# Optimization experiments

Hardware: AMD Instinct MI355X
Metric: run time of the kernel (lower is better)

## Reference

```python
import math
import jax, jax.numpy as jnp
import numpy as np

EPS = 1e-7
MAX_TANH_ARG = 1.0 - 1e-5

def _norm(x):
    return jnp.sqrt(jnp.sum(x * x, axis=-1, keepdims=True)).clip(EPS)

def logmap0(x):  # Poincare ball, c=1
    n = _norm(x)
    return jnp.arctanh(jnp.clip(n, EPS, MAX_TANH_ARG)) * x / n

def expmap0(v):
    n = _norm(v)
    return jnp.tanh(n) * v / n

def mobius_add(x, y):
    x2 = jnp.sum(x * x, -1, keepdims=True)
    y2 = jnp.sum(y * y, -1, keepdims=True)
    xy = jnp.sum(x * y, -1, keepdims=True)
    num = (1 + 2 * xy + y2) * x + (1 - x2) * y
    den = (1 + 2 * xy + x2 * y2).clip(EPS)
    return num / den

def plin(x, w, b):  # PoincareLinear: tangent-space affine map
    return expmap0(logmap0(x) @ w + b)

def layer_norm(x, eps=1e-6):  # elementwise_affine=False
    m = x.mean(-1, keepdims=True)
    v = ((x - m) ** 2).mean(-1, keepdims=True)
    return (x - m) / jnp.sqrt(v + eps)

def _beta(a, b):
    return math.exp(math.lgamma(a) + math.lgamma(b) - math.lgamma(a + b))

D, H, FF = 1024, 16, 4096
HD = D // H
BETA_N = _beta(D / 2, 0.5)   # beta(n/2, 1/2) for full dim
BETA_H = _beta(HD / 2, 0.5)  # beta(ni/2, 1/2) for head dim


def setup_inputs() -> dict:
    key = jax.random.key(0)
    ks = jax.random.split(key, 20)
    B, S = 4, 1024
    x = expmap0(0.02 * jax.random.normal(ks[0], (B, S, D), jnp.float32))
    t_emb = jax.random.normal(ks[1], (B, 1, D), jnp.float32)
    g = lambda k, sh: 0.02 * jax.random.normal(k, sh, jnp.float32)
    return {
        'x': x, 't_emb': t_emb,
        'w_q': g(ks[2], (D, D)), 'b_q': jnp.zeros((D,), jnp.float32),
        'w_k': g(ks[3], (D, D)), 'b_k': jnp.zeros((D,), jnp.float32),
        'w_v': g(ks[4], (D, D)), 'b_v': jnp.zeros((D,), jnp.float32),
        'w_o': g(ks[5], (D, D)), 'b_o': jnp.zeros((D,), jnp.float32),
        'w_f1': g(ks[6], (D, FF)), 'b_f1': jnp.zeros((FF,), jnp.float32),
        'w_f2': g(ks[7], (FF, D)), 'b_f2': jnp.zeros((D,), jnp.float32),
        'w_ada': g(ks[8], (D, 6 * D)), 'b_ada': jnp.zeros((6 * D,), jnp.float32),
    }


def _to_heads(p):
    # beta-split: logmap0, split per head, scale by beta_ni/beta_n, expmap0
    B, S, _ = p.shape
    t = logmap0(p).reshape(B, S, H, HD) * (BETA_H / BETA_N)
    return expmap0(jnp.transpose(t, (0, 2, 1, 3)))  # [B,H,S,HD]


def _from_heads(ph):
    # beta-concat: logmap0 per head, scale by beta_n/beta_ni, concat, expmap0
    B, _, S, _ = ph.shape
    t = logmap0(ph) * (BETA_N / BETA_H)
    t = jnp.transpose(t, (0, 2, 1, 3)).reshape(B, S, D)
    return expmap0(t)


def reference(x, t_emb, w_q, b_q, w_k, b_k, w_v, b_v, w_o, b_o,
              w_f1, b_f1, w_f2, b_f2, w_ada, b_ada):
    ada = t_emb @ w_ada + b_ada  # [B,1,6D]
    sh_msa, sc_msa, g_msa, sh_mlp, sc_mlp, g_mlp = jnp.split(ada, 6, axis=-1)

    # --- attention block ---
    residual = x
    xn = layer_norm(logmap0(x))
    xm = expmap0(xn * (1 + sc_msa) + sh_msa)

    q = _to_heads(plin(xm, w_q, b_q))
    k = _to_heads(plin(xm, w_k, b_k))
    v = _to_heads(plin(xm, w_v, b_v))

    qt, kt, vt = logmap0(q), logmap0(k), logmap0(v)
    scores = jnp.einsum('bhqd,bhkd->bhqk', qt, kt) / math.sqrt(HD)
    attn = jax.nn.softmax(scores, axis=-1)
    out_h = expmap0(jnp.einsum('bhqk,bhkd->bhqd', attn, vt))  # [B,H,S,HD]

    attn_out = plin(_from_heads(out_h), w_o, b_o)
    attn_t = g_msa * logmap0(attn_out)
    x = mobius_add(residual, expmap0(attn_t))

    # --- FFN block ---
    residual = x
    xn = layer_norm(logmap0(x))
    xm = expmap0(xn * (1 + sc_mlp) + sh_mlp)
    ff = plin(plin(xm, w_f1, b_f1), w_f2, b_f2)
    ff_t = g_mlp * logmap0(ff)
    return mobius_add(residual, expmap0(ff_t))
```

## Files before the change

kernel.cpp:

```cpp
#include <hip/hip_runtime.h>
#include <cmath>


constexpr int kD  = 1024;
constexpr int kH  = 16;
constexpr int kHD = 64;
constexpr int kFF = 4096;
constexpr int kB  = 4;
constexpr int kS  = 1024;
constexpr int kN  = kB * kS;

#define EPSF 1e-7f
#define MTAF (1.0f - 1e-5f)
#define LOG2E 1.4426950408889634f

typedef unsigned int uint32;
typedef unsigned short ushort16;
typedef __attribute__((ext_vector_type(8))) short short8x;
typedef __attribute__((ext_vector_type(4))) float floatx4;

__device__ __forceinline__ ushort16 f2b(float f) {
  union { float f; uint32 u; } x; x.f = f;
  uint32 r = x.u + 0x7fffu + ((x.u >> 16) & 1u);
  return (ushort16)(r >> 16);
}
__device__ __forceinline__ float b2f(ushort16 u) {
  union { uint32 u; float f; } x; x.u = ((uint32)u) << 16;
  return x.f;
}
__device__ __forceinline__ void load_b4(const ushort16* p, float v[4]) {
  uint2 u = *(const uint2*)p;
  v[0] = b2f((ushort16)(u.x & 0xffff)); v[1] = b2f((ushort16)(u.x >> 16));
  v[2] = b2f((ushort16)(u.y & 0xffff)); v[3] = b2f((ushort16)(u.y >> 16));
}
__device__ __forceinline__ void store_b4(ushort16* p, const float v[4]) {
  uint2 u;
  u.x = (uint32)f2b(v[0]) | ((uint32)f2b(v[1]) << 16);
  u.y = (uint32)f2b(v[2]) | ((uint32)f2b(v[3]) << 16);
  *(uint2*)p = u;
}

__device__ __forceinline__ float atanh_clipped(float n) {
  float c = fminf(n, MTAF);
  return 0.5f * logf((1.0f + c) / (1.0f - c));
}
__device__ __forceinline__ float logmap0_scale(float nraw) {
  float n = fmaxf(nraw, EPSF);
  return atanh_clipped(n) / n;
}
__device__ __forceinline__ float expmap0_scale(float nraw) {
  float n = fmaxf(nraw, EPSF);
  return tanhf(n) / n;
}
__device__ __forceinline__ float roundtrip_scale(float nraw) {
  float nu = fmaxf(nraw, EPSF);
  float se = tanhf(nu) / nu;
  float nb = fmaxf(se * nraw, EPSF);
  float sl = atanh_clipped(nb) / nb;
  return sl * se;
}

__device__ __forceinline__ float blockReduceSum256(float v, float* s4) {
#pragma unroll
  for (int o = 32; o > 0; o >>= 1) v += __shfl_xor(v, o);
  int wave = threadIdx.x >> 6;
  if ((threadIdx.x & 63) == 0) s4[wave] = v;
  __syncthreads();
  float r = s4[0] + s4[1] + s4[2] + s4[3];
  __syncthreads();
  return r;
}
__device__ __forceinline__ float redSum16(float v) {
#pragma unroll
  for (int o = 8; o > 0; o >>= 1) v += __shfl_xor(v, o);
  return v;
}

__device__ __forceinline__ void async16(const void* g, void* l) {
  __builtin_amdgcn_global_load_lds(
      (const __attribute__((address_space(1))) uint32*)g,
      (__attribute__((address_space(3))) uint32*)l, 16, 0, 0);
}

__device__ __forceinline__ void transpose_tile(const float* __restrict__ src,
                                               ushort16* __restrict__ dst,
                                               int K, int N, int n0, int k0) {
  __shared__ float T[64][65];
  int tid = threadIdx.x;
#pragma unroll
  for (int p = 0; p < 4; ++p) {
    int idx = p * 1024 + tid * 4;
    int r = idx >> 6, c = idx & 63;
    float4 t = *(const float4*)&src[(size_t)(k0 + r) * N + n0 + c];
    T[r][c] = t.x; T[r][c + 1] = t.y; T[r][c + 2] = t.z; T[r][c + 3] = t.w;
  }
  __syncthreads();
#pragma unroll
  for (int p = 0; p < 4; ++p) {
    int idx = p * 1024 + tid * 4;
    int r = idx >> 6, c = idx & 63;
    float v[4] = {T[c][r], T[c + 1][r], T[c + 2][r], T[c + 3][r]};
    store_b4(&dst[(size_t)(n0 + r) * K + k0 + c], v);
  }
}
__global__ __launch_bounds__(256) void k_transpose_bf16(const float* __restrict__ src,
                                                        ushort16* __restrict__ dst,
                                                        int K, int N) {
  transpose_tile(src, dst, K, N, blockIdx.x * 64, blockIdx.y * 64);
}
__global__ __launch_bounds__(256) void k_transpose4(
    const float* __restrict__ s0, const float* __restrict__ s1,
    const float* __restrict__ s2, const float* __restrict__ s3,
    ushort16* __restrict__ d0, ushort16* __restrict__ d1,
    ushort16* __restrict__ d2, ushort16* __restrict__ d3) {
  const float* src = (blockIdx.z == 0) ? s0 : (blockIdx.z == 1) ? s1
                    : (blockIdx.z == 2) ? s2 : s3;
  ushort16* dst = (blockIdx.z == 0) ? d0 : (blockIdx.z == 1) ? d1
                 : (blockIdx.z == 2) ? d2 : d3;
  transpose_tile(src, dst, kD, kD, blockIdx.x * 64, blockIdx.y * 64);
}

__global__ __launch_bounds__(256) void k_ada(const float* __restrict__ t_emb,
                                             const float* __restrict__ w_ada,
                                             const float* __restrict__ b_ada,
                                             float* __restrict__ ada) {
  __shared__ float te[kD];
  __shared__ float part[4][64];
  int b = blockIdx.y;
  int tid = threadIdx.x;
  {
    float4 t = *(const float4*)&t_emb[b * kD + tid * 4];
    te[tid * 4] = t.x; te[tid * 4 + 1] = t.y; te[tid * 4 + 2] = t.z; te[tid * 4 + 3] = t.w;
  }
  __syncthreads();
  int c = tid & 63, kc = tid >> 6;
  int col = blockIdx.x * 64 + c;
  float acc = 0.f;
#pragma unroll 8
  for (int k = kc * 256; k < kc * 256 + 256; ++k)
    acc += te[k] * w_ada[(size_t)k * (6 * kD) + col];
  part[kc][c] = acc;
  __syncthreads();
  if (tid < 64)
    ada[b * 6 * kD + blockIdx.x * 64 + tid] =
        part[0][tid] + part[1][tid] + part[2][tid] + part[3][tid] +
        b_ada[blockIdx.x * 64 + tid];
}

__global__ __launch_bounds__(256) void k_prenorm(const float* __restrict__ x,
                                                 const float* __restrict__ ada,
                                                 int sh_off, int sc_off,
                                                 ushort16* __restrict__ out) {
  __shared__ float sred[4];
  int tok = blockIdx.x;
  int b = tok >> 10;
  int d4 = threadIdx.x * 4;
  float xv[4];
  *(float4*)xv = *(const float4*)&x[(size_t)tok * kD + d4];
  float ss = xv[0] * xv[0] + xv[1] * xv[1] + xv[2] * xv[2] + xv[3] * xv[3];
  ss = blockReduceSum256(ss, sred);
  float sl = logmap0_scale(sqrtf(ss));
  float sum = 0.f;
#pragma unroll
  for (int i = 0; i < 4; ++i) { xv[i] *= sl; sum += xv[i]; }
  sum = blockReduceSum256(sum, sred);
  float mean = sum * (1.0f / kD);
  float vs = 0.f;
#pragma unroll
  for (int i = 0; i < 4; ++i) { xv[i] -= mean; vs += xv[i] * xv[i]; }
  vs = blockReduceSum256(vs, sred);
  float inv = rsqrtf(vs * (1.0f / kD) + 1e-6f);
  float shv[4], scv[4];
  *(float4*)shv = *(const float4*)&ada[b * 6 * kD + sh_off + d4];
  *(float4*)scv = *(const float4*)&ada[b * 6 * kD + sc_off + d4];
  float uu = 0.f;
#pragma unroll
  for (int i = 0; i < 4; ++i) {
    float u = xv[i] * inv * (1.0f + scv[i]) + shv[i];
    xv[i] = u;
    uu += u * u;
  }
  uu = blockReduceSum256(uu, sred);
  float s = roundtrip_scale(sqrtf(uu));
#pragma unroll
  for (int i = 0; i < 4; ++i) xv[i] *= s;
  store_b4(out + (size_t)tok * kD + d4, xv);
}

template <int OUT_BF16, int KSPLIT>
__global__ __launch_bounds__(256, 2) void k_gemm_bf16(
    const ushort16* __restrict__ A,
    const ushort16* __restrict__ Bt0, const ushort16* __restrict__ Bt1,
    const ushort16* __restrict__ Bt2,
    const float* __restrict__ bias0, const float* __restrict__ bias1,
    const float* __restrict__ bias2,
    const float* __restrict__ rowscale,
    void* __restrict__ C0, void* __restrict__ C1, void* __restrict__ C2,
    int M, int N, int K) {
  const ushort16* Bt;
  const float* bias;
  void* C;
  int k_lo, k_hi;
  bool add_bias;
  if (KSPLIT == 1) {
    Bt = (blockIdx.z == 0) ? Bt0 : ((blockIdx.z == 1) ? Bt1 : Bt2);
    bias = (blockIdx.z == 0) ? bias0 : ((blockIdx.z == 1) ? bias1 : bias2);
    C = (blockIdx.z == 0) ? C0 : ((blockIdx.z == 1) ? C1 : C2);
    k_lo = 0; k_hi = K; add_bias = true;
  } else {
    Bt = Bt0; bias = bias0;
    C = (blockIdx.z == 0) ? C0 : C1;
    int kchunk = K / KSPLIT;
    k_lo = blockIdx.z * kchunk; k_hi = k_lo + kchunk;
    add_bias = (blockIdx.z == 0);
  }

  __shared__ __align__(16) ushort16 As[2 * 128 * 64];
  __shared__ __align__(16) ushort16 Bs[2 * 128 * 64];

  int tid = threadIdx.x;
  int lane = tid & 63;
  int wave = tid >> 6;
  int wr = (wave >> 1) & 1, wc = wave & 1;
  int c16 = lane & 15, quad = lane >> 4;
  int row0 = blockIdx.x * 128, col0 = blockIdx.y * 128;

  int srow = tid >> 3;
  int scol = (((tid & 7) ^ ((tid >> 4) & 7)) << 3);
  const ushort16* a_src = A + (size_t)(row0 + srow) * K + k_lo + scol;
  const ushort16* b_src = Bt + (size_t)(col0 + srow) * K + k_lo + scol;
  int sdst = tid * 8;
  int nt = (k_hi - k_lo) >> 6;

  auto stage = [&](int tt) {
    int cc = tt & 1;
    size_t ko = (size_t)tt * 64;
#pragma unroll
    for (int p = 0; p < 4; ++p) {
      async16(a_src + ko + (size_t)(p * 32) * K, (ushort16*)As + cc * 8192 + p * 2048 + sdst);
      async16(b_src + ko + (size_t)(p * 32) * K, (ushort16*)Bs + cc * 8192 + p * 2048 + sdst);
    }
  };

  int xsw = (c16 >> 1) & 7;
  int aoff0 = (wr * 64 + c16) * 64 + ((quad ^ xsw) << 3);
  int aoff1 = (wr * 64 + c16) * 64 + (((4 + quad) ^ xsw) << 3);
  int boff0 = (wc * 64 + c16) * 64 + ((quad ^ xsw) << 3);
  int boff1 = (wc * 64 + c16) * 64 + (((4 + quad) ^ xsw) << 3);

  floatx4 acc[4][4];
#pragma unroll
  for (int i = 0; i < 4; ++i)
#pragma unroll
    for (int j = 0; j < 4; ++j) acc[i][j] = (floatx4)0.f;

  stage(0);
  stage(1);
  asm volatile("s_waitcnt vmcnt(8)" ::: "memory");
  __builtin_amdgcn_s_barrier();

  for (int t = 0; t < nt; ++t) {
    int cc = t & 1;
    const ushort16* Ab = (const ushort16*)As + cc * 8192;
    const ushort16* Bb = (const ushort16*)Bs + cc * 8192;
    short8x a[4][2], b[4][2];
#pragma unroll
    for (int i = 0; i < 4; ++i) {
      a[i][0] = *(const short8x*)&Ab[i * 1024 + aoff0];
      a[i][1] = *(const short8x*)&Ab[i * 1024 + aoff1];
      b[i][0] = *(const short8x*)&Bb[i * 1024 + boff0];
      b[i][1] = *(const short8x*)&Bb[i * 1024 + boff1];
    }
    __builtin_amdgcn_s_setprio(1);
#pragma unroll
    for (int i = 0; i < 4; ++i)
#pragma unroll
      for (int j = 0; j < 4; ++j)
        acc[i][j] = __builtin_amdgcn_mfma_f32_16x16x32_bf16(a[i][0], b[j][0], acc[i][j], 0, 0, 0);
    __builtin_amdgcn_s_setprio(0);
    asm volatile("s_waitcnt lgkmcnt(0)" ::: "memory");
    __builtin_amdgcn_s_barrier();
    if (t + 2 < nt) stage(t + 2);
    __builtin_amdgcn_s_setprio(1);
#pragma unroll
    for (int i = 0; i < 4; ++i)
#pragma unroll
      for (int j = 0; j < 4; ++j)
        acc[i][j] = __builtin_amdgcn_mfma_f32_16x16x32_bf16(a[i][1], b[j][1], acc[i][j], 0, 0, 0);
    __builtin_amdgcn_s_setprio(0);
    if (t + 2 < nt) {
      asm volatile("s_waitcnt vmcnt(8)" ::: "memory");
    } else {
      asm volatile("s_waitcnt vmcnt(0)" ::: "memory");
    }
    __builtin_amdgcn_s_barrier();
  }

  float bv[4];
#pragma unroll
  for (int j = 0; j < 4; ++j)
    bv[j] = add_bias ? bias[col0 + wc * 64 + j * 16 + c16] : 0.f;
  int rowq = quad * 4;
#pragma unroll
  for (int i = 0; i < 4; ++i) {
    int rbase = row0 + wr * 64 + i * 16 + rowq;
    float rs4[4];
#pragma unroll
    for (int r = 0; r < 4; ++r) rs4[r] = rowscale ? rowscale[rbase + r] : 1.0f;
#pragma unroll
    for (int j = 0; j < 4; ++j) {
      int c = col0 + wc * 64 + j * 16 + c16;
#pragma unroll
      for (int r = 0; r < 4; ++r) {
        float v = acc[i][j][r] * rs4[r] + bv[j];
        if (KSPLIT == 2) {
          if (blockIdx.z == 0) ((float*)C)[(size_t)(rbase + r) * N + c] = v;
          else ((ushort16*)C)[(size_t)(rbase + r) * N + c] = f2b(v);
        } else if (OUT_BF16) {
          ((ushort16*)C)[(size_t)(rbase + r) * N + c] = f2b(v);
        } else {
          ((float*)C)[(size_t)(rbase + r) * N + c] = v;
        }
      }
    }
  }
}

__global__ __launch_bounds__(256) void k_headsplit_b(const ushort16* __restrict__ q_in,
                                                     ushort16* __restrict__ k_io,
                                                     ushort16* __restrict__ v_io,
                                                     ushort16* __restrict__ qb_out,
                                                     float ratio) {
  __shared__ float sred[4];
  int tok = blockIdx.x;
  int tid = threadIdx.x;
  int d4 = tid * 4;
#pragma unroll
  for (int t = 0; t < 3; ++t) {
    const ushort16* p = (t == 0 ? q_in : (t == 1 ? (const ushort16*)k_io
                                                 : (const ushort16*)v_io)) +
                        (size_t)tok * kD + d4;
    float val[4];
    load_b4(p, val);
    float psq = val[0] * val[0] + val[1] * val[1] + val[2] * val[2] + val[3] * val[3];
    float hsq = redSum16(psq);
    float tot = blockReduceSum256(psq, sred);
    float s1 = roundtrip_scale(sqrtf(tot));
    float c = s1 * ratio;
    float s2 = roundtrip_scale(c * sqrtf(hsq));
    float f = c * s2 * (t == 0 ? (0.125f * LOG2E) : 1.0f);
#pragma unroll
    for (int i = 0; i < 4; ++i) val[i] *= f;
    ushort16* op = (t == 0 ? qb_out : (t == 1 ? k_io : v_io)) + (size_t)tok * kD + d4;
    store_b4(op, val);
    __syncthreads();
  }
}

__global__ __launch_bounds__(256) void k_vtrans_b(const ushort16* __restrict__ v,
                                                  ushort16* __restrict__ vT) {
  __shared__ ushort16 T[64][68];
  int bh = blockIdx.y, b = bh >> 4, h = bh & 15;
  int s0 = blockIdx.x * 64;
  int tid = threadIdx.x;
#pragma unroll
  for (int p = 0; p < 4; ++p) {
    int idx = p * 1024 + tid * 4;
    int r = idx >> 6, d = idx & 63;
    *(uint2*)&T[r][d] = *(const uint2*)&v[(size_t)(b * kS + s0 + r) * kD + h * kHD + d];
  }
  __syncthreads();
#pragma unroll
  for (int p = 0; p < 16; ++p) {
    int idx = p * 256 + tid;
    int d = idx >> 6, c = idx & 63;
    int cp = (c & 32) | ((c & 15) << 1) | ((c >> 4) & 1);
    vT[((size_t)bh * kHD + d) * kS + s0 + cp] = T[c][d];
  }
}

__global__ __launch_bounds__(256) void k_attn_mfma(ushort16* __restrict__ qb,
                                                   const ushort16* __restrict__ kb,
                                                   const ushort16* __restrict__ vT,
                                                   float ratio2) {
  __shared__ __align__(16) ushort16 Ks[2 * 2 * 128 * 32];
  __shared__ __align__(16) ushort16 Vs[4 * 64 * 32];
  __shared__ __align__(16) ushort16 Ps[4 * 4 * 16 * 40];
  int bh = blockIdx.x, b = bh >> 4, h = bh & 15;
  int q0 = blockIdx.y * 128;
  int tid = threadIdx.x, lane = tid & 63, wave = tid >> 6;
  int c16 = lane & 15, quad = lane >> 4;
  int sw = (lane >> 1) & 3;
  int cbp = ((quad ^ sw) << 3);
  int wq = wave * 32;
  constexpr int NT = kS / 128;

  short8x a_q[2][2];
#pragma unroll
  for (int i = 0; i < 2; ++i)
#pragma unroll
    for (int kk = 0; kk < 2; ++kk)
      a_q[i][kk] = *(const short8x*)&qb[(size_t)(b * kS + q0 + wq + i * 16 + c16) * kD +
                                        h * kHD + kk * 32 + quad * 8];

  short8x ones;
#pragma unroll
  for (int j = 0; j < 8; ++j) ones[j] = (short)0x3F80;

  floatx4 o[2][4], ol[2];
#pragma unroll
  for (int i = 0; i < 2; ++i) {
    ol[i] = (floatx4)0.f;
#pragma unroll
    for (int n = 0; n < 4; ++n) o[i][n] = (floatx4)0.f;
  }

  const ushort16* kbase = kb + ((size_t)b * kS) * kD + h * kHD;
  const ushort16* vbase = vT + (size_t)bh * kHD * kS;

  auto stageK = [&](int t) {
    int cbuf = t & 1;
#pragma unroll
    for (int tt = 0; tt < 2; ++tt)
#pragma unroll
      for (int cb2 = 0; cb2 < 2; ++cb2) {
        int e = cb2 * 2048 + tid * 8;
        int key = e >> 5;
        int col = ((((e >> 3) & 3) ^ ((key >> 1) & 3)) << 3);
        async16(kbase + (size_t)(t * 128 + key) * kD + tt * 32 + col,
                Ks + cbuf * 8192 + tt * 4096 + e);
      }
  };
  auto stageV = [&](int t) {
#pragma unroll
    for (int tt = 0; tt < 4; ++tt) {
      int e = tid * 8;
      int dd = e >> 5;
      int col = ((((e >> 3) & 3) ^ ((dd >> 1) & 3)) << 3);
      async16(vbase + (size_t)dd * kS + t * 128 + tt * 32 + col, Vs + tt * 2048 + e);
    }
  };

  stageK(0);
  stageV(0);
  stageK(1);
  asm volatile("s_waitcnt vmcnt(8)" ::: "memory");
  __builtin_amdgcn_s_barrier();

  for (int t = 0; t < NT; ++t) {
    const ushort16* Kc = (const ushort16*)Ks + (t & 1) * 8192;

#pragma unroll
    for (int i = 0; i < 2; ++i) {
      floatx4 s[8];
#pragma unroll
      for (int n = 0; n < 8; ++n) s[n] = (floatx4)0.f;
      __builtin_amdgcn_s_setprio(1);
#pragma unroll
      for (int kkd = 0; kkd < 2; ++kkd)
#pragma unroll
        for (int n = 0; n < 8; ++n) {
          short8x bk = *(const short8x*)&Kc[kkd * 4096 + (n * 16 + c16) * 32 + cbp];
          s[n] = __builtin_amdgcn_mfma_f32_16x16x32_bf16(a_q[i][kkd], bk, s[n], 0, 0, 0);
        }
      __builtin_amdgcn_s_setprio(0);

#pragma unroll
      for (int r = 0; r < 4; ++r) {
#pragma unroll
        for (int j = 0; j < 4; ++j) {
          float e0 = exp2f(s[2 * j][r]);
          float e1 = exp2f(s[2 * j + 1][r]);
          uint32 u;
          asm("v_cvt_pk_bf16_f32 %0, %1, %2" : "=v"(u) : "v"(e0), "v"(e1));
          *(uint32*)&Ps[(((wave * 4 + j) * 16) + (quad * 4 + r)) * 40 + c16 * 2] = u;
        }
      }

      if (i == 0) {
        if (t + 1 < NT) {
          asm volatile("s_waitcnt vmcnt(4)" ::: "memory");
        } else {
          asm volatile("s_waitcnt vmcnt(0)" ::: "memory");
        }
        __builtin_amdgcn_s_barrier();
      }

      __builtin_amdgcn_s_setprio(1);
#pragma unroll
      for (int kk = 0; kk < 4; ++kk) {
        short8x ap = *(const short8x*)&Ps[(((wave * 4 + kk) * 16) + c16) * 40 + quad * 8];
#pragma unroll
        for (int n = 0; n < 4; ++n) {
          short8x bv = *(const short8x*)&Vs[kk * 2048 + (n * 16 + c16) * 32 + cbp];
          o[i][n] = __builtin_amdgcn_mfma_f32_16x16x32_bf16(ap, bv, o[i][n], 0, 0, 0);
        }
        ol[i] = __builtin_amdgcn_mfma_f32_16x16x32_bf16(ap, ones, ol[i], 0, 0, 0);
      }
      __builtin_amdgcn_s_setprio(0);
    }

    asm volatile("s_waitcnt lgkmcnt(0)" ::: "memory");
    __builtin_amdgcn_s_barrier();
    if (t + 1 < NT) stageV(t + 1);
    if (t + 2 < NT) stageK(t + 2);
    if (t + 2 < NT) {
      asm volatile("s_waitcnt vmcnt(8)" ::: "memory");
    } else if (t + 1 < NT) {
      asm volatile("s_waitcnt vmcnt(4)" ::: "memory");
    } else {
      asm volatile("s_waitcnt vmcnt(0)" ::: "memory");
    }
    __builtin_amdgcn_s_barrier();
  }

#pragma unroll
  for (int i = 0; i < 2; ++i)
#pragma unroll
    for (int r = 0; r < 4; ++r) {
      float invl = 1.0f / ol[i][r];
      float w[4];
      float pssq = 0.f;
#pragma unroll
      for (int n = 0; n < 4; ++n) { w[n] = o[i][n][r] * invl; pssq += w[n] * w[n]; }
      float ssq = redSum16(pssq);
      float coef = roundtrip_scale(sqrtf(ssq)) * ratio2;
      int row = b * kS + q0 + wq + i * 16 + quad * 4 + r;
#pragma unroll
      for (int n = 0; n < 4; ++n)
        qb[(size_t)row * kD + h * kHD + n * 16 + c16] = f2b(coef * w[n]);
    }
}

template <int WIDTH>
__global__ __launch_bounds__(256) void k_rowscale(const ushort16* __restrict__ p,
                                                  float* __restrict__ s) {
  __shared__ float sred[4];
  constexpr int PER = WIDTH / 1024;
  size_t base = (size_t)blockIdx.x * WIDTH;
  float ss = 0.f;
#pragma unroll
  for (int i = 0; i < PER; ++i) {
    float v[4];
    load_b4(p + base + i * 1024 + threadIdx.x * 4, v);
    ss += v[0] * v[0] + v[1] * v[1] + v[2] * v[2] + v[3] * v[3];
  }
  ss = blockReduceSum256(ss, sred);
  if (threadIdx.x == 0) s[blockIdx.x] = roundtrip_scale(sqrtf(ss));
}

__device__ __forceinline__ void mobius_body(float xv[4], float tv[4],
                                            const float* gp, int d4,
                                            float* sred, float outv[4]) {
  float ss = tv[0] * tv[0] + tv[1] * tv[1] + tv[2] * tv[2] + tv[3] * tv[3];
  ss = blockReduceSum256(ss, sred);
  float s5 = roundtrip_scale(sqrtf(ss));
  float gv[4];
  *(float4*)gv = *(const float4*)&gp[d4];
  float at2 = 0.f;
#pragma unroll
  for (int i = 0; i < 4; ++i) {
    float a = gv[i] * s5 * tv[i];
    tv[i] = a;
    at2 += a * a;
  }
  at2 = blockReduceSum256(at2, sred);
  float nyraw = sqrtf(at2);
  float sy = expmap0_scale(nyraw);
  float ynorm = sy * nyraw;
  float y2 = ynorm * ynorm;
  float x2p = 0.f, xyp = 0.f;
#pragma unroll
  for (int i = 0; i < 4; ++i) {
    float y = sy * tv[i];
    tv[i] = y;
    x2p += xv[i] * xv[i];
    xyp += xv[i] * y;
  }
  float x2 = blockReduceSum256(x2p, sred);
  float xy = blockReduceSum256(xyp, sred);
  float cx = 1.0f + 2.0f * xy + y2;
  float cy = 1.0f - x2;
  float den = fmaxf(1.0f + 2.0f * xy + x2 * y2, EPSF);
  float invden = 1.0f / den;
#pragma unroll
  for (int i = 0; i < 4; ++i) outv[i] = (cx * xv[i] + cy * tv[i]) * invden;
}

__global__ __launch_bounds__(256) void k_epilogue2(const float* __restrict__ xres,
                                                   const float* __restrict__ ot0,
                                                   const ushort16* __restrict__ ot1b,
                                                   const float* __restrict__ ada,
                                                   int g_off,
                                                   float* __restrict__ out) {
  __shared__ float sred[4];
  int tok = blockIdx.x;
  int b = tok >> 10;
  size_t base = (size_t)tok * kD;
  int d4 = threadIdx.x * 4;
  float xv[4], tv[4], t1[4];
  *(float4*)tv = *(const float4*)&ot0[base + d4];
  load_b4(ot1b + base + d4, t1);
  *(float4*)xv = *(const float4*)&xres[base + d4];
#pragma unroll
  for (int i = 0; i < 4; ++i) tv[i] += t1[i];
  float outv[4];
  mobius_body(xv, tv, ada + b * 6 * kD + g_off, d4, sred, outv);
  *(float4*)&out[base + d4] = *(float4*)outv;
}

__global__ __launch_bounds__(256) void k_epi_pre(const float* __restrict__ xres,
                                                 const float* __restrict__ ot0,
                                                 const ushort16* __restrict__ ot1b,
                                                 const float* __restrict__ ada,
                                                 float* __restrict__ xmid_out,
                                                 ushort16* __restrict__ lx2_out) {
  __shared__ float sred[4];
  int tok = blockIdx.x;
  int b = tok >> 10;
  size_t base = (size_t)tok * kD;
  int d4 = threadIdx.x * 4;
  float xv[4], tv[4], t1[4];
  *(float4*)tv = *(const float4*)&ot0[base + d4];
  load_b4(ot1b + base + d4, t1);
  *(float4*)xv = *(const float4*)&xres[base + d4];
#pragma unroll
  for (int i = 0; i < 4; ++i) tv[i] += t1[i];
  float xm[4];
  mobius_body(xv, tv, ada + b * 6 * kD + 2 * kD, d4, sred, xm);
  *(float4*)&xmid_out[base + d4] = *(float4*)xm;

  float ss = xm[0] * xm[0] + xm[1] * xm[1] + xm[2] * xm[2] + xm[3] * xm[3];
  ss = blockReduceSum256(ss, sred);
  float sl = logmap0_scale(sqrtf(ss));
  float sum = 0.f;
#pragma unroll
  for (int i = 0; i < 4; ++i) { xm[i] *= sl; sum += xm[i]; }
  sum = blockReduceSum256(sum, sred);
  float mean = sum * (1.0f / kD);
  float vs = 0.f;
#pragma unroll
  for (int i = 0; i < 4; ++i) { xm[i] -= mean; vs += xm[i] * xm[i]; }
  vs = blockReduceSum256(vs, sred);
  float inv = rsqrtf(vs * (1.0f / kD) + 1e-6f);
  float shv[4], scv[4];
  *(float4*)shv = *(const float4*)&ada[b * 6 * kD + 3 * kD + d4];
  *(float4*)scv = *(const float4*)&ada[b * 6 * kD + 4 * kD + d4];
  float uu = 0.f;
#pragma unroll
  for (int i = 0; i < 4; ++i) {
    float u = xm[i] * inv * (1.0f + scv[i]) + shv[i];
    xm[i] = u;
    uu += u * u;
  }
  uu = blockReduceSum256(uu, sred);
  float s = roundtrip_scale(sqrtf(uu));
#pragma unroll
  for (int i = 0; i < 4; ++i) xm[i] *= s;
  store_b4(lx2_out + base + d4, xm);
}

extern "C" void kernel_launch(void* const* d_in, const int* in_sizes, int n_in,
                              void* d_out, int out_size, void* d_ws, size_t ws_size,
                              hipStream_t stream) {
  const float* x     = (const float*)d_in[0];
  const float* t_emb = (const float*)d_in[1];
  const float* w_q = (const float*)d_in[2];  const float* b_q = (const float*)d_in[3];
  const float* w_k = (const float*)d_in[4];  const float* b_k = (const float*)d_in[5];
  const float* w_v = (const float*)d_in[6];  const float* b_v = (const float*)d_in[7];
  const float* w_o = (const float*)d_in[8];  const float* b_o = (const float*)d_in[9];
  const float* w_f1 = (const float*)d_in[10]; const float* b_f1 = (const float*)d_in[11];
  const float* w_f2 = (const float*)d_in[12]; const float* b_f2 = (const float*)d_in[13];
  const float* w_ada = (const float*)d_in[14]; const float* b_ada = (const float*)d_in[15];
  float* out = (float*)d_out;

  constexpr size_t ND = (size_t)kN * kD;
  constexpr size_t NF = (size_t)kN * kFF;
  constexpr size_t DD = (size_t)kD * kD;

  float* ws   = (float*)d_ws;
  float* ada  = ws;
  float* qt   = ada + 6 * kD * kB;
  float* kt   = qt + ND;
  float* vt   = kt + ND;
  ushort16* qbA = (ushort16*)(vt + ND);
  ushort16* kb  = qbA + ND;
  ushort16* vTb = kb + ND;
  ushort16* actB = vTb + ND;
  ushort16* wqT  = actB + NF;
  ushort16* wkT  = wqT + DD;
  ushort16* wvT  = wkT + DD;
  ushort16* woT  = wvT + DD;
  ushort16* wf1T = woT + DD;
  ushort16* wf2T = wf1T + (size_t)kD * kFF;

  double bn = exp(lgamma(512.0) + lgamma(0.5) - lgamma(512.5));
  double bh = exp(lgamma(32.0) + lgamma(0.5) - lgamma(32.5));
  float R1 = (float)(bh / bn);
  float R2 = (float)(bn / bh);

  k_transpose4<<<dim3(16, 16, 4), 256, 0, stream>>>(w_q, w_k, w_v, w_o,
                                                    wqT, wkT, wvT, woT);
  k_transpose_bf16<<<dim3(64, 16), 256, 0, stream>>>(w_f1, wf1T, kD, kFF);
  k_transpose_bf16<<<dim3(16, 64), 256, 0, stream>>>(w_f2, wf2T, kFF, kD);
  k_ada<<<dim3(6 * kD / 64, kB), 256, 0, stream>>>(t_emb, w_ada, b_ada, ada);
  k_prenorm<<<kN, 256, 0, stream>>>(x, ada, 0 * kD, 1 * kD, qbA);
  k_gemm_bf16<1, 1><<<dim3(kN / 128, kD / 128, 3), 256, 0, stream>>>(
      qbA, wqT, wkT, wvT, b_q, b_k, b_v, nullptr, kb, vTb, actB, kN, kD, kD);
  k_headsplit_b<<<kN, 256, 0, stream>>>(kb, vTb, actB, qbA, R1);
  k_vtrans_b<<<dim3(kS / 64, kB * kH), 256, 0, stream>>>(actB, kb);
  k_attn_mfma<<<dim3(kB * kH, kS / 128), 256, 0, stream>>>(qbA, vTb, kb, R2);
  k_rowscale<kD><<<kN, 256, 0, stream>>>(qbA, kt);
  k_gemm_bf16<0, 2><<<dim3(kN / 128, kD / 128, 2), 256, 0, stream>>>(
      qbA, woT, woT, woT, b_o, b_o, b_o, kt, qt, kb, nullptr, kN, kD, kD);
  k_epi_pre<<<kN, 256, 0, stream>>>(x, qt, kb, ada, vt, qbA);
  k_gemm_bf16<1, 1><<<dim3(kN / 128, kFF / 128, 1), 256, 0, stream>>>(
      qbA, wf1T, wf1T, wf1T, b_f1, b_f1, b_f1, nullptr, actB, actB, actB, kN, kFF, kD);
  k_rowscale<kFF><<<kN, 256, 0, stream>>>(actB, kt);
  k_gemm_bf16<0, 2><<<dim3(kN / 128, kD / 128, 2), 256, 0, stream>>>(
      actB, wf2T, wf2T, wf2T, b_f2, b_f2, b_f2, kt, qt, kb, nullptr, kN, kD, kFF);
  k_epilogue2<<<kN, 256, 0, stream>>>(vt, qt, kb, ada, 5 * kD, out);

  (void)in_sizes; (void)n_in; (void)out_size; (void)ws_size;
}
```

Before: 409.3 us.

## Load GEMM A operand directly into registers, bypassing LDS staging

The GEMM kernel no longer stages the A tile through shared memory. Each wave now loads its A fragments straight from global memory into registers, double-buffered one k-tile ahead, while B keeps the async LDS double buffer. The main loop is restructured into two alternating steps with a sched_barrier, and both MFMA halves now run back to back. This aims to cut LDS traffic and one barrier per iteration, but A is now read redundantly by the two column waves with less-coalesced per-lane 16-byte loads. The loop also assumes an even tile count and relies on compiler-inserted vmcnt waits to make B visible in LDS.

```diff
diff --git a/kernel.cpp b/kernel.cpp
--- a/kernel.cpp
+++ b/kernel.cpp
@@ -215,7 +215,6 @@
     add_bias = (blockIdx.z == 0);
   }
 
-  __shared__ __align__(16) ushort16 As[2 * 128 * 64];
   __shared__ __align__(16) ushort16 Bs[2 * 128 * 64];
 
   int tid = threadIdx.x;
@@ -227,73 +226,79 @@
 
   int srow = tid >> 3;
   int scol = (((tid & 7) ^ ((tid >> 4) & 7)) << 3);
-  const ushort16* a_src = A + (size_t)(row0 + srow) * K + k_lo + scol;
   const ushort16* b_src = Bt + (size_t)(col0 + srow) * K + k_lo + scol;
   int sdst = tid * 8;
   int nt = (k_hi - k_lo) >> 6;
 
-  auto stage = [&](int tt) {
+  auto stageB = [&](int tt) {
     int cc = tt & 1;
     size_t ko = (size_t)tt * 64;
 #pragma unroll
-    for (int p = 0; p < 4; ++p) {
-      async16(a_src + ko + (size_t)(p * 32) * K, (ushort16*)As + cc * 8192 + p * 2048 + sdst);
+    for (int p = 0; p < 4; ++p)
       async16(b_src + ko + (size_t)(p * 32) * K, (ushort16*)Bs + cc * 8192 + p * 2048 + sdst);
+  };
+
+  int xsw = (c16 >> 1) & 7;
+  int boff0 = (wc * 64 + c16) * 64 + ((quad ^ xsw) << 3);
+  int boff1 = (wc * 64 + c16) * 64 + (((4 + quad) ^ xsw) << 3);
+
+  const ushort16* a_base[4];
+#pragma unroll
+  for (int i = 0; i < 4; ++i)
+    a_base[i] = A + (size_t)(row0 + wr * 64 + i * 16 + c16) * K + k_lo + quad * 8;
+
+  short8x aA[4][2], aB[4][2];
+  auto loadA = [&](short8x (&dst)[4][2], int tt) {
+    size_t off = (size_t)tt * 64;
+#pragma unroll
+    for (int i = 0; i < 4; ++i) {
+      dst[i][0] = *(const short8x*)(a_base[i] + off);
+      dst[i][1] = *(const short8x*)(a_base[i] + off + 32);
     }
   };
 
-  int xsw = (c16 >> 1) & 7;
-  int aoff0 = (wr * 64 + c16) * 64 + ((quad ^ xsw) << 3);
-  int aoff1 = (wr * 64 + c16) * 64 + (((4 + quad) ^ xsw) << 3);
-  int boff0 = (wc * 64 + c16) * 64 + ((quad ^ xsw) << 3);
-  int boff1 = (wc * 64 + c16) * 64 + (((4 + quad) ^ xsw) << 3);
-
   floatx4 acc[4][4];
 #pragma unroll
   for (int i = 0; i < 4; ++i)
 #pragma unroll
     for (int j = 0; j < 4; ++j) acc[i][j] = (floatx4)0.f;
 
-  stage(0);
-  stage(1);
-  asm volatile("s_waitcnt vmcnt(8)" ::: "memory");
+  stageB(0);
+  stageB(1);
+  loadA(aA, 0);
+  asm volatile("s_waitcnt vmcnt(0)" ::: "memory");
   __builtin_amdgcn_s_barrier();
 
-  for (int t = 0; t < nt; ++t) {
-    int cc = t & 1;
-    const ushort16* Ab = (const ushort16*)As + cc * 8192;
-    const ushort16* Bb = (const ushort16*)Bs + cc * 8192;
-    short8x a[4][2], b[4][2];
-#pragma unroll
-    for (int i = 0; i < 4; ++i) {
-      a[i][0] = *(const short8x*)&Ab[i * 1024 + aoff0];
-      a[i][1] = *(const short8x*)&Ab[i * 1024 + aoff1];
-      b[i][0] = *(const short8x*)&Bb[i * 1024 + boff0];
-      b[i][1] = *(const short8x*)&Bb[i * 1024 + boff1];
+  auto step = [&](int t, short8x (&cur)[4][2], short8x (&nxt)[4][2]) {
+    const ushort16* Bb = (const ushort16*)Bs + (t & 1) * 8192;
+    short8x b[4][2];
+#pragma unroll
+    for (int j = 0; j < 4; ++j) {
+      b[j][0] = *(const short8x*)&Bb[j * 1024 + boff0];
+      b[j][1] = *(const short8x*)&Bb[j * 1024 + boff1];
     }
     __builtin_amdgcn_s_setprio(1);
 #pragma unroll
     for (int i = 0; i < 4; ++i)
 #pragma unroll
       for (int j = 0; j < 4; ++j)
-        acc[i][j] = __builtin_amdgcn_mfma_f32_16x16x32_bf16(a[i][0], b[j][0], acc[i][j], 0, 0, 0);
+        acc[i][j] = __builtin_amdgcn_mfma_f32_16x16x32_bf16(cur[i][0], b[j][0], acc[i][j], 0, 0, 0);
+#pragma unroll
+    for (int i = 0; i < 4; ++i)
+#pragma unroll
+      for (int j = 0; j < 4; ++j)
+        acc[i][j] = __builtin_amdgcn_mfma_f32_16x16x32_bf16(cur[i][1], b[j][1], acc[i][j], 0, 0, 0);
     __builtin_amdgcn_s_setprio(0);
     asm volatile("s_waitcnt lgkmcnt(0)" ::: "memory");
     __builtin_amdgcn_s_barrier();
-    if (t + 2 < nt) stage(t + 2);
-    __builtin_amdgcn_s_setprio(1);
-#pragma unroll
-    for (int i = 0; i < 4; ++i)
-#pragma unroll
-      for (int j = 0; j < 4; ++j)
-        acc[i][j] = __builtin_amdgcn_mfma_f32_16x16x32_bf16(a[i][1], b[j][1], acc[i][j], 0, 0, 0);
-    __builtin_amdgcn_s_setprio(0);
-    if (t + 2 < nt) {
-      asm volatile("s_waitcnt vmcnt(8)" ::: "memory");
-    } else {
-      asm volatile("s_waitcnt vmcnt(0)" ::: "memory");
-    }
-    __builtin_amdgcn_s_barrier();
+    if (t + 2 < nt) stageB(t + 2);
+    __builtin_amdgcn_sched_barrier(0);
+    if (t + 1 < nt) loadA(nxt, t + 1);
+  };
+
+  for (int t = 0; t < nt; t += 2) {
+    step(t, aA, aB);
+    step(t + 1, aB, aA);
   }
 
   float bv[4];
```

Measured after the change: 548.8 us. 1.34x slower.

## Fuse row sum-of-squares into GEMM and attention epilogues; swizzle GEMM block order

Applied to the files above, without the earlier changes.

The separate k_rowscale passes, which reread the attention output and the 4096-wide FFN activation, are removed. Per-row squared norms are now accumulated with atomics in the epilogues of the attention kernel and the FF1 GEMM. A small k_rtfinal kernel turns each accumulated norm into a scale and resets the accumulator. The GEMM also remaps block indices with an 8-way swizzle meant to improve L2 reuse. This trades extra atomics, epilogue work and two tiny launches for avoiding a full read of the activations.

```diff
diff --git a/kernel.cpp b/kernel.cpp
--- a/kernel.cpp
+++ b/kernel.cpp
@@ -145,6 +145,16 @@
     ada[b * 6 * kD + blockIdx.x * 64 + tid] =
         part[0][tid] + part[1][tid] + part[2][tid] + part[3][tid] +
         b_ada[blockIdx.x * 64 + tid];
+}
+
+__global__ __launch_bounds__(256) void k_zero(float* __restrict__ p) {
+  p[blockIdx.x * 256 + threadIdx.x] = 0.f;
+}
+__global__ __launch_bounds__(256) void k_rtfinal(float* __restrict__ ssq,
+                                                 float* __restrict__ scale) {
+  int i = blockIdx.x * 256 + threadIdx.x;
+  scale[i] = roundtrip_scale(sqrtf(ssq[i]));
+  ssq[i] = 0.f;
 }
 
 __global__ __launch_bounds__(256) void k_prenorm(const float* __restrict__ x,
@@ -195,6 +205,7 @@
     const float* __restrict__ bias0, const float* __restrict__ bias1,
     const float* __restrict__ bias2,
     const float* __restrict__ rowscale,
+    float* __restrict__ ssq_out,
     void* __restrict__ C0, void* __restrict__ C1, void* __restrict__ C2,
     int M, int N, int K) {
   const ushort16* Bt;
@@ -223,7 +234,12 @@
   int wave = tid >> 6;
   int wr = (wave >> 1) & 1, wc = wave & 1;
   int c16 = lane & 15, quad = lane >> 4;
-  int row0 = blockIdx.x * 128, col0 = blockIdx.y * 128;
+
+  int lin = blockIdx.y * gridDim.x + blockIdx.x;
+  int nwg = gridDim.x * gridDim.y;
+  int swz = (lin & 7) * (nwg >> 3) + (lin >> 3);
+  int bx = swz % gridDim.x, by = swz / gridDim.x;
+  int row0 = bx * 128, col0 = by * 128;
 
   int srow = tid >> 3;
   int scol = (((tid & 7) ^ ((tid >> 4) & 7)) << 3);
@@ -307,6 +323,7 @@
     float rs4[4];
 #pragma unroll
     for (int r = 0; r < 4; ++r) rs4[r] = rowscale ? rowscale[rbase + r] : 1.0f;
+    float srow4[4] = {0.f, 0.f, 0.f, 0.f};
 #pragma unroll
     for (int j = 0; j < 4; ++j) {
       int c = col0 + wc * 64 + j * 16 + c16;
@@ -317,10 +334,21 @@
           if (blockIdx.z == 0) ((float*)C)[(size_t)(rbase + r) * N + c] = v;
           else ((ushort16*)C)[(size_t)(rbase + r) * N + c] = f2b(v);
         } else if (OUT_BF16) {
-          ((ushort16*)C)[(size_t)(rbase + r) * N + c] = f2b(v);
+          ushort16 ub = f2b(v);
+          ((ushort16*)C)[(size_t)(rbase + r) * N + c] = ub;
+          if (ssq_out) { float vr = b2f(ub); srow4[r] += vr * vr; }
         } else {
           ((float*)C)[(size_t)(rbase + r) * N + c] = v;
         }
+      }
+    }
+    if (OUT_BF16 && KSPLIT == 1 && ssq_out) {
+#pragma unroll
+      for (int r = 0; r < 4; ++r) {
+        float s = srow4[r];
+#pragma unroll
+        for (int o = 8; o > 0; o >>= 1) s += __shfl_xor(s, o);
+        if (c16 == 0) atomicAdd(&ssq_out[rbase + r], s);
       }
     }
   }
@@ -382,7 +410,8 @@
 __global__ __launch_bounds__(256) void k_attn_mfma(ushort16* __restrict__ qb,
                                                    const ushort16* __restrict__ kb,
                                                    const ushort16* __restrict__ vT,
-                                                   float ratio2) {
+                                                   float ratio2,
+                                                   float* __restrict__ ssq) {
   __shared__ __align__(16) ushort16 Ks[2 * 2 * 128 * 32];
   __shared__ __align__(16) ushort16 Vs[4 * 64 * 32];
   __shared__ __align__(16) ushort16 Ps[4 * 4 * 16 * 40];
@@ -523,30 +552,20 @@
       float pssq = 0.f;
 #pragma unroll
       for (int n = 0; n < 4; ++n) { w[n] = o[i][n][r] * invl; pssq += w[n] * w[n]; }
-      float ssq = redSum16(pssq);
-      float coef = roundtrip_scale(sqrtf(ssq)) * ratio2;
+      float sq = redSum16(pssq);
+      float coef = roundtrip_scale(sqrtf(sq)) * ratio2;
       int row = b * kS + q0 + wq + i * 16 + quad * 4 + r;
-#pragma unroll
-      for (int n = 0; n < 4; ++n)
-        qb[(size_t)row * kD + h * kHD + n * 16 + c16] = f2b(coef * w[n]);
-    }
-}
-
-template <int WIDTH>
-__global__ __launch_bounds__(256) void k_rowscale(const ushort16* __restrict__ p,
-                                                  float* __restrict__ s) {
-  __shared__ float sred[4];
-  constexpr int PER = WIDTH / 1024;
-  size_t base = (size_t)blockIdx.x * WIDTH;
-  float ss = 0.f;
-#pragma unroll
-  for (int i = 0; i < PER; ++i) {
-    float v[4];
-    load_b4(p + base + i * 1024 + threadIdx.x * 4, v);
-    ss += v[0] * v[0] + v[1] * v[1] + v[2] * v[2] + v[3] * v[3];
-  }
-  ss = blockReduceSum256(ss, sred);
-  if (threadIdx.x == 0) s[blockIdx.x] = roundtrip_scale(sqrtf(ss));
+      float ts = 0.f;
+#pragma unroll
+      for (int n = 0; n < 4; ++n) {
+        ushort16 ub = f2b(coef * w[n]);
+        qb[(size_t)row * kD + h * kHD + n * 16 + c16] = ub;
+        float vv = b2f(ub);
+        ts += vv * vv;
+      }
+      ts = redSum16(ts);
+      if (c16 == 0) atomicAdd(&ssq[row], ts);
+    }
 }
 
 __device__ __forceinline__ void mobius_body(float xv[4], float tv[4],
@@ -693,12 +712,14 @@
   ushort16* woT  = wvT + DD;
   ushort16* wf1T = woT + DD;
   ushort16* wf2T = wf1T + (size_t)kD * kFF;
+  float* ssq = (float*)(wf2T + (size_t)kFF * kD);
 
   double bn = exp(lgamma(512.0) + lgamma(0.5) - lgamma(512.5));
   double bh = exp(lgamma(32.0) + lgamma(0.5) - lgamma(32.5));
   float R1 = (float)(bh / bn);
   float R2 = (float)(bn / bh);
 
+  k_zero<<<kN / 256, 256, 0, stream>>>(ssq);
   k_transpose4<<<dim3(16, 16, 4), 256, 0, stream>>>(w_q, w_k, w_v, w_o,
                                                     wqT, wkT, wvT, woT);
   k_transpose_bf16<<<dim3(64, 16), 256, 0, stream>>>(w_f1, wf1T, kD, kFF);
@@ -706,19 +727,19 @@
   k_ada<<<dim3(6 * kD / 64, kB), 256, 0, stream>>>(t_emb, w_ada, b_ada, ada);
   k_prenorm<<<kN, 256, 0, stream>>>(x, ada, 0 * kD, 1 * kD, qbA);
   k_gemm_bf16<1, 1><<<dim3(kN / 128, kD / 128, 3), 256, 0, stream>>>(
-      qbA, wqT, wkT, wvT, b_q, b_k, b_v, nullptr, kb, vTb, actB, kN, kD, kD);
+      qbA, wqT, wkT, wvT, b_q, b_k, b_v, nullptr, nullptr, kb, vTb, actB, kN, kD, kD);
   k_headsplit_b<<<kN, 256, 0, stream>>>(kb, vTb, actB, qbA, R1);
   k_vtrans_b<<<dim3(kS / 64, kB * kH), 256, 0, stream>>>(actB, kb);
-  k_attn_mfma<<<dim3(kB * kH, kS / 128), 256, 0, stream>>>(qbA, vTb, kb, R2);
-  k_rowscale<kD><<<kN, 256, 0, stream>>>(qbA, kt);
+  k_attn_mfma<<<dim3(kB * kH, kS / 128), 256, 0, stream>>>(qbA, vTb, kb, R2, ssq);
+  k_rtfinal<<<kN / 256, 256, 0, stream>>>(ssq, kt);
   k_gemm_bf16<0, 2><<<dim3(kN / 128, kD / 128, 2), 256, 0, stream>>>(
-      qbA, woT, woT, woT, b_o, b_o, b_o, kt, qt, kb, nullptr, kN, kD, kD);
+      qbA, woT, woT, woT, b_o, b_o, b_o, kt, nullptr, qt, kb, nullptr, kN, kD, kD);
   k_epi_pre<<<kN, 256, 0, stream>>>(x, qt, kb, ada, vt, qbA);
   k_gemm_bf16<1, 1><<<dim3(kN / 128, kFF / 128, 1), 256, 0, stream>>>(
-      qbA, wf1T, wf1T, wf1T, b_f1, b_f1, b_f1, nullptr, actB, actB, actB, kN, kFF, kD);
-  k_rowscale<kFF><<<kN, 256, 0, stream>>>(actB, kt);
+      qbA, wf1T, wf1T, wf1T, b_f1, b_f1, b_f1, nullptr, ssq, actB, actB, actB, kN, kFF, kD);
+  k_rtfinal<<<kN / 256, 256, 0, stream>>>(ssq, kt);
   k_gemm_bf16<0, 2><<<dim3(kN / 128, kD / 128, 2), 256, 0, stream>>>(
-      actB, wf2T, wf2T, wf2T, b_f2, b_f2, b_f2, kt, qt, kb, nullptr, kN, kD, kFF);
+      actB, wf2T, wf2T, wf2T, b_f2, b_f2, b_f2, kt, nullptr, qt, kb, nullptr, kN, kD, kFF);
   k_epilogue2<<<kN, 256, 0, stream>>>(vt, qt, kb, ada, 5 * kD, out);
 
   (void)in_sizes; (void)n_in; (void)out_size; (void)ws_size;
```

Result: slower. 453.3 us (+10.8%).
